# Kernel optimization log

Hardware: AMD Instinct MI355X
Metric: run time of the kernel (lower is better)

The kernel has to match this reference:

```python
import jax, jax.numpy as jnp
import numpy as np

H = 1024
NH = 16
DH = H // NH

def setup_inputs() -> dict:
    key = jax.random.key(0)
    ks = jax.random.split(key, 6)
    s = 1.0 / np.sqrt(H)
    x = jax.random.normal(ks[0], (4, 2048, H), dtype=jnp.float32)
    Wq = jax.random.uniform(ks[1], (H, H), jnp.float32, -s, s)
    Wk = jax.random.uniform(ks[2], (H, H), jnp.float32, -s, s)
    Wv = jax.random.uniform(ks[3], (H, H), jnp.float32, -s, s)
    Wo = jax.random.uniform(ks[4], (H, H), jnp.float32, -s, s)
    bo = jax.random.uniform(ks[5], (H,), jnp.float32, -s, s)
    return {"x": x, "Wq": Wq, "Wk": Wk, "Wv": Wv, "Wo": Wo, "bo": bo}

def reference(x, Wq, Wk, Wv, Wo, bo):
    B, T, Hd = x.shape
    # projections: torch Linear is x @ W.T
    def split_heads(y):
        return y.reshape(B, T, NH, DH).transpose(0, 2, 1, 3)  # [B, nh, T, dh]
    Q = split_heads(x @ Wq.T)
    K = split_heads(x @ Wk.T)
    V = split_heads(x @ Wv.T)
    scores = jnp.einsum('bhtd,bhsd->bhts', Q, K) / jnp.sqrt(jnp.float32(DH))
    w = jax.nn.softmax(scores, axis=-1)
    ctx = jnp.einsum('bhts,bhsd->bhtd', w, V)  # [B, nh, T, dh]
    ctx = ctx.transpose(0, 2, 1, 3).reshape(B, T, Hd)
    out = ctx @ Wo.T + bo  # [B, T, H]
    return out.mean(axis=1)  # [B, H]
```

## Files before the change

### kernel.cpp

```cpp
#include <hip/hip_runtime.h>
#include <hip/hip_bf16.h>
#include <cstdint>

#define BB   4
#define TT   2048
#define HH   1024
#define NHH  16
#define DHH  64
#define MM   (BB*TT)
#define N3   (3*HH)

typedef __attribute__((ext_vector_type(8))) short short8;
typedef __attribute__((ext_vector_type(4))) float f32x4;

__device__ __forceinline__ float bf2f(unsigned short u) {
    return __uint_as_float(((uint32_t)u) << 16);
}
__device__ __forceinline__ unsigned short f2bf(float f) {
    uint32_t u = __float_as_uint(f);
    return (unsigned short)((u + 0x7fffu + ((u >> 16) & 1u)) >> 16);
}
__device__ __forceinline__ void gload_lds16(const unsigned short* g, unsigned short* l) {
    __builtin_amdgcn_global_load_lds(
        (const __attribute__((address_space(1))) uint32_t*)g,
        (__attribute__((address_space(3))) uint32_t*)l, 16, 0, 0);
}

__global__ __launch_bounds__(256) void cvt_bf16(
    const float* __restrict__ src, unsigned short* __restrict__ dst, int n4)
{
    int i = blockIdx.x * 256 + threadIdx.x;
    const int stride = gridDim.x * 256;
    for (; i < n4; i += stride) {
        float4 v = ((const float4*)src)[i];
        ushort4 o;
        o.x = f2bf(v.x); o.y = f2bf(v.y); o.z = f2bf(v.z); o.w = f2bf(v.w);
        ((ushort4*)dst)[i] = o;
    }
}

__global__ __launch_bounds__(256) void proj_mfma(
    const unsigned short* __restrict__ xb, const unsigned short* __restrict__ Wb,
    unsigned short* __restrict__ C)
{
    __shared__ unsigned short As[4096];
    __shared__ unsigned short Bs[4096];
    const int m0 = blockIdx.x * 128;
    const int n0 = blockIdx.y * 128;
    const unsigned short* Wbase = Wb + (size_t)(n0 >> 10) * HH * HH;
    const int nw0 = n0 & (HH - 1);
    const int tid = threadIdx.x;
    const int wave = tid >> 6, lane = tid & 63;
    const int quad = lane >> 4, l15 = lane & 15;
    const int wm = wave >> 1, wn = wave & 1;

    f32x4 acc[4][4];
    #pragma unroll
    for (int i = 0; i < 4; ++i)
        #pragma unroll
        for (int j = 0; j < 4; ++j) acc[i][j] = (f32x4){0.f, 0.f, 0.f, 0.f};

    for (int k0 = 0; k0 < HH; k0 += 32) {
        __syncthreads();
        #pragma unroll
        for (int q = 0; q < 2; ++q) {
            const int chunk = (wave * 2 + q) * 64 + lane;
            const int kc = chunk >> 7, mrow = chunk & 127;
            gload_lds16(xb    + (size_t)(m0  + mrow) * HH + k0 + kc * 8, As + chunk * 8);
            gload_lds16(Wbase + (size_t)(nw0 + mrow) * HH + k0 + kc * 8, Bs + chunk * 8);
        }
        __syncthreads();
        short8 af[4], bf[4];
        #pragma unroll
        for (int i = 0; i < 4; ++i)
            af[i] = *(const short8*)&As[(quad * 128 + wm * 64 + i * 16 + l15) * 8];
        #pragma unroll
        for (int j = 0; j < 4; ++j)
            bf[j] = *(const short8*)&Bs[(quad * 128 + wn * 64 + j * 16 + l15) * 8];
        #pragma unroll
        for (int i = 0; i < 4; ++i)
            #pragma unroll
            for (int j = 0; j < 4; ++j)
                acc[i][j] = __builtin_amdgcn_mfma_f32_16x16x32_bf16(af[i], bf[j], acc[i][j], 0, 0, 0);
    }
    const float cscale = (n0 < HH) ? 0.125f : 1.0f;
    #pragma unroll
    for (int i = 0; i < 4; ++i)
        #pragma unroll
        for (int j = 0; j < 4; ++j) {
            const int col = n0 + wn * 64 + j * 16 + l15;
            #pragma unroll
            for (int r = 0; r < 4; ++r) {
                const int row = m0 + wm * 64 + i * 16 + quad * 4 + r;
                C[(size_t)row * N3 + col] = f2bf(acc[i][j][r] * cscale);
            }
        }
}

__global__ __launch_bounds__(256) void attn_fused(
    const unsigned short* __restrict__ qkv, float* __restrict__ a)
{
    const int t0 = blockIdx.x * 128;
    const int h = blockIdx.y, b = blockIdx.z;
    const int tid = threadIdx.x;
    const int wave = tid >> 6, lane = tid & 63;
    const int quad = lane >> 4, l15 = lane & 15;
    const int bh = b * NHH + h;
    __shared__ float red[4][128];
    __shared__ float linv[128];

    const size_t qbase = (size_t)(b * TT) * N3 + h * DHH;
    const size_t kbase = qbase + HH;

    short8 aq[8][2];
    #pragma unroll
    for (int i = 0; i < 8; ++i)
        #pragma unroll
        for (int c = 0; c < 2; ++c)
            aq[i][c] = *(const short8*)&qkv[qbase + (size_t)(t0 + i * 16 + l15) * N3 + quad * 8 + c * 32];

    float rs[8][4];
    #pragma unroll
    for (int i = 0; i < 8; ++i)
        #pragma unroll
        for (int r = 0; r < 4; ++r) rs[i][r] = 0.f;

    const size_t kstripe = kbase + (size_t)(wave * 512 + l15) * N3 + quad * 8;
    short8 nb0 = *(const short8*)&qkv[kstripe];
    short8 nb1 = *(const short8*)&qkv[kstripe + 32];
    for (int sstep = 0; sstep < 32; ++sstep) {
        const short8 bq0 = nb0, bq1 = nb1;
        if (sstep < 31) {
            const size_t krow = kstripe + (size_t)((sstep + 1) * 16) * N3;
            nb0 = *(const short8*)&qkv[krow];
            nb1 = *(const short8*)&qkv[krow + 32];
        }
        #pragma unroll
        for (int i = 0; i < 8; ++i) {
            f32x4 c = (f32x4){0.f, 0.f, 0.f, 0.f};
            c = __builtin_amdgcn_mfma_f32_16x16x32_bf16(aq[i][0], bq0, c, 0, 0, 0);
            c = __builtin_amdgcn_mfma_f32_16x16x32_bf16(aq[i][1], bq1, c, 0, 0, 0);
            #pragma unroll
            for (int r = 0; r < 4; ++r) rs[i][r] += __expf(c[r]);
        }
    }
    #pragma unroll
    for (int off = 1; off < 16; off <<= 1)
        #pragma unroll
        for (int i = 0; i < 8; ++i)
            #pragma unroll
            for (int r = 0; r < 4; ++r) rs[i][r] += __shfl_xor(rs[i][r], off);
    if (l15 == 0)
        #pragma unroll
        for (int i = 0; i < 8; ++i)
            #pragma unroll
            for (int r = 0; r < 4; ++r) red[wave][i * 16 + quad * 4 + r] = rs[i][r];
    __syncthreads();
    if (tid < 128) {
        const float l = red[0][tid] + red[1][tid] + red[2][tid] + red[3][tid];
        linv[tid] = 1.0f / (l * (float)TT);
    }
    __syncthreads();

    float lrv[8][4];
    #pragma unroll
    for (int i = 0; i < 8; ++i)
        #pragma unroll
        for (int r = 0; r < 4; ++r) lrv[i][r] = linv[i * 16 + quad * 4 + r];

    nb0 = *(const short8*)&qkv[kstripe];
    nb1 = *(const short8*)&qkv[kstripe + 32];
    for (int sstep = 0; sstep < 32; ++sstep) {
        const short8 bq0 = nb0, bq1 = nb1;
        if (sstep < 31) {
            const size_t krow = kstripe + (size_t)((sstep + 1) * 16) * N3;
            nb0 = *(const short8*)&qkv[krow];
            nb1 = *(const short8*)&qkv[krow + 32];
        }
        float cs = 0.f;
        #pragma unroll
        for (int i = 0; i < 8; ++i) {
            f32x4 c = (f32x4){0.f, 0.f, 0.f, 0.f};
            c = __builtin_amdgcn_mfma_f32_16x16x32_bf16(aq[i][0], bq0, c, 0, 0, 0);
            c = __builtin_amdgcn_mfma_f32_16x16x32_bf16(aq[i][1], bq1, c, 0, 0, 0);
            #pragma unroll
            for (int r = 0; r < 4; ++r) cs += __expf(c[r]) * lrv[i][r];
        }
        cs += __shfl_xor(cs, 16);
        cs += __shfl_xor(cs, 32);
        if (lane < 16)
            atomicAdd(&a[(size_t)bh * TT + wave * 512 + sstep * 16 + l15], cs);
    }
}

__global__ __launch_bounds__(256) void ctx_mean(
    const unsigned short* __restrict__ qkv, const float* __restrict__ a,
    float* __restrict__ cm)
{
    const int h = blockIdx.x, b = blockIdx.y, sb = blockIdx.z;
    const int tid = threadIdx.x;
    const int d = tid & 63, sg = tid >> 6;
    __shared__ float red[4][64];
    float part = 0.f;
    for (int s = sb * 256 + sg; s < sb * 256 + 256; s += 4) {
        const float av = a[(size_t)(b * NHH + h) * TT + s];
        part += av * bf2f(qkv[(size_t)(b * TT + s) * N3 + 2 * HH + h * DHH + d]);
    }
    red[sg][d] = part;
    __syncthreads();
    if (tid < 64)
        atomicAdd(&cm[b * HH + h * DHH + tid],
                  red[0][tid] + red[1][tid] + red[2][tid] + red[3][tid]);
}

__global__ __launch_bounds__(256) void out_proj(
    const float* __restrict__ cm, const float* __restrict__ Wo,
    const float* __restrict__ bo, float* __restrict__ out)
{
    const int b = blockIdx.y;
    const int jb = blockIdx.x;
    const int tid = threadIdx.x;
    const int j = jb * 64 + (tid >> 2);
    const int kg = tid & 3;
    __shared__ float cs[HH];
    for (int k = tid; k < HH; k += 256) cs[k] = cm[b * HH + k];
    __syncthreads();
    float acc = 0.f;
    const float* wrow = &Wo[(size_t)j * HH];
    #pragma unroll 8
    for (int i = 0; i < 64; ++i) {
        const int k = kg * 256 + i * 4;
        float4 w4 = *(const float4*)&wrow[k];
        acc += w4.x * cs[k] + w4.y * cs[k+1] + w4.z * cs[k+2] + w4.w * cs[k+3];
    }
    acc += __shfl_down(acc, 2, 4);
    acc += __shfl_down(acc, 1, 4);
    if (kg == 0) out[b * HH + j] = acc + bo[j];
}

extern "C" void kernel_launch(void* const* d_in, const int* in_sizes, int n_in,
                              void* d_out, int out_size, void* d_ws, size_t ws_size,
                              hipStream_t stream) {
    const float* x  = (const float*)d_in[0];
    const float* Wq = (const float*)d_in[1];
    const float* Wk = (const float*)d_in[2];
    const float* Wv = (const float*)d_in[3];
    const float* Wo = (const float*)d_in[4];
    const float* bo = (const float*)d_in[5];
    float* out = (float*)d_out;

    char* ws = (char*)d_ws;
    unsigned short* qkv = (unsigned short*)ws;
    ws += (size_t)MM * N3 * 2;
    unsigned short* xb = (unsigned short*)ws;
    ws += (size_t)MM * HH * 2;
    unsigned short* Wb = (unsigned short*)ws;
    ws += (size_t)3 * HH * HH * 2;
    float* a = (float*)ws;
    ws += (size_t)BB * NHH * TT * 4;
    float* cm = (float*)ws;

    hipMemsetAsync(a, 0, (size_t)(BB * NHH * TT + BB * HH) * 4, stream);

    cvt_bf16<<<2048, 256, 0, stream>>>(x,  xb,           MM * HH / 4);
    cvt_bf16<<<512,  256, 0, stream>>>(Wq, Wb,           HH * HH / 4);
    cvt_bf16<<<512,  256, 0, stream>>>(Wk, Wb + HH*HH,   HH * HH / 4);
    cvt_bf16<<<512,  256, 0, stream>>>(Wv, Wb + 2*HH*HH, HH * HH / 4);

    proj_mfma <<<dim3(64, 24),      256, 0, stream>>>(xb, Wb, qkv);
    attn_fused<<<dim3(16, NHH, BB), 256, 0, stream>>>(qkv, a);
    ctx_mean  <<<dim3(NHH, BB, 8),  256, 0, stream>>>(qkv, a, cm);
    out_proj  <<<dim3(16, BB),      256, 0, stream>>>(cm, Wo, bo, out);
}
```

Before: 335.5 us.

## Store Q/K/V head-major, use exp2 with folded log2e scale, deepen K prefetch

The projection epilogue now writes Q, K and V into separate [B,NH,T,DH] buffers instead of one interleaved [M,3H] matrix, so the attention and ctx kernels read contiguous per-head rows. The Q scale folds in log2(e), which lets the softmax use the hardware exp2 instead of __expf. The K register prefetch is deepened to two steps ahead, and the three weight conversions are merged into one launch. In exchange, the projection's scattered epilogue stores may coalesce less well, and the extra prefetch registers raise register pressure.

```diff
diff --git a/kernel.cpp b/kernel.cpp
--- a/kernel.cpp
+++ b/kernel.cpp
@@ -13,6 +13,14 @@
 typedef __attribute__((ext_vector_type(8))) short short8;
 typedef __attribute__((ext_vector_type(4))) float f32x4;
 
+#if __has_builtin(__builtin_amdgcn_exp2f)
+#define EXP2F(x) __builtin_amdgcn_exp2f(x)
+#else
+#define EXP2F(x) exp2f(x)
+#endif
+
+#define QSCALE 0.1803368801111204f
+
 __device__ __forceinline__ float bf2f(unsigned short u) {
     return __uint_as_float(((uint32_t)u) << 16);
 }
@@ -39,15 +47,34 @@
     }
 }
 
+__global__ __launch_bounds__(256) void cvt_w3(
+    const float* __restrict__ Wq, const float* __restrict__ Wk,
+    const float* __restrict__ Wv, unsigned short* __restrict__ Wb)
+{
+    const float* src = (blockIdx.y == 0) ? Wq : (blockIdx.y == 1 ? Wk : Wv);
+    unsigned short* dst = Wb + (size_t)blockIdx.y * HH * HH;
+    const int n4 = HH * HH / 4;
+    int i = blockIdx.x * 256 + threadIdx.x;
+    const int stride = gridDim.x * 256;
+    for (; i < n4; i += stride) {
+        float4 v = ((const float4*)src)[i];
+        ushort4 o;
+        o.x = f2bf(v.x); o.y = f2bf(v.y); o.z = f2bf(v.z); o.w = f2bf(v.w);
+        ((ushort4*)dst)[i] = o;
+    }
+}
+
 __global__ __launch_bounds__(256) void proj_mfma(
     const unsigned short* __restrict__ xb, const unsigned short* __restrict__ Wb,
-    unsigned short* __restrict__ C)
+    unsigned short* __restrict__ qp, unsigned short* __restrict__ kp,
+    unsigned short* __restrict__ vp)
 {
     __shared__ unsigned short As[4096];
     __shared__ unsigned short Bs[4096];
     const int m0 = blockIdx.x * 128;
     const int n0 = blockIdx.y * 128;
-    const unsigned short* Wbase = Wb + (size_t)(n0 >> 10) * HH * HH;
+    const int sel = n0 >> 10;
+    const unsigned short* Wbase = Wb + (size_t)sel * HH * HH;
     const int nw0 = n0 & (HH - 1);
     const int tid = threadIdx.x;
     const int wave = tid >> 6, lane = tid & 63;
@@ -83,41 +110,50 @@
             for (int j = 0; j < 4; ++j)
                 acc[i][j] = __builtin_amdgcn_mfma_f32_16x16x32_bf16(af[i], bf[j], acc[i][j], 0, 0, 0);
     }
-    const float cscale = (n0 < HH) ? 0.125f : 1.0f;
+    unsigned short* outp = (sel == 0) ? qp : (sel == 1 ? kp : vp);
+    const float cscale = (sel == 0) ? QSCALE : 1.0f;
     #pragma unroll
     for (int i = 0; i < 4; ++i)
         #pragma unroll
         for (int j = 0; j < 4; ++j) {
             const int col = n0 + wn * 64 + j * 16 + l15;
+            const int hh2 = (col >> 6) & (NHH - 1);
+            const int dd  = col & (DHH - 1);
             #pragma unroll
             for (int r = 0; r < 4; ++r) {
                 const int row = m0 + wm * 64 + i * 16 + quad * 4 + r;
-                C[(size_t)row * N3 + col] = f2bf(acc[i][j][r] * cscale);
+                const int bb2 = row >> 11, tt2 = row & (TT - 1);
+                outp[((size_t)(bb2 * NHH + hh2) * TT + tt2) * DHH + dd] =
+                    f2bf(acc[i][j][r] * cscale);
             }
         }
 }
 
 __global__ __launch_bounds__(256) void attn_fused(
-    const unsigned short* __restrict__ qkv, float* __restrict__ a)
+    const unsigned short* __restrict__ qp, const unsigned short* __restrict__ kp,
+    float* __restrict__ a)
 {
     const int t0 = blockIdx.x * 128;
     const int h = blockIdx.y, b = blockIdx.z;
+    const int bh = b * NHH + h;
     const int tid = threadIdx.x;
     const int wave = tid >> 6, lane = tid & 63;
     const int quad = lane >> 4, l15 = lane & 15;
-    const int bh = b * NHH + h;
     __shared__ float red[4][128];
     __shared__ float linv[128];
 
-    const size_t qbase = (size_t)(b * TT) * N3 + h * DHH;
-    const size_t kbase = qbase + HH;
+    const unsigned short* q = qp + (size_t)bh * TT * DHH;
+    const unsigned short* kptr =
+        kp + (size_t)bh * TT * DHH + (size_t)(wave * 512 + l15) * DHH + quad * 8;
 
     short8 aq[8][2];
     #pragma unroll
     for (int i = 0; i < 8; ++i)
         #pragma unroll
         for (int c = 0; c < 2; ++c)
-            aq[i][c] = *(const short8*)&qkv[qbase + (size_t)(t0 + i * 16 + l15) * N3 + quad * 8 + c * 32];
+            aq[i][c] = *(const short8*)&q[(size_t)(t0 + i * 16 + l15) * DHH + quad * 8 + c * 32];
+
+#define KLD(ss, c) (*(const short8*)(kptr + (size_t)(ss) * 16 * DHH + (c) * 32))
 
     float rs[8][4];
     #pragma unroll
@@ -125,23 +161,21 @@
         #pragma unroll
         for (int r = 0; r < 4; ++r) rs[i][r] = 0.f;
 
-    const size_t kstripe = kbase + (size_t)(wave * 512 + l15) * N3 + quad * 8;
-    short8 nb0 = *(const short8*)&qkv[kstripe];
-    short8 nb1 = *(const short8*)&qkv[kstripe + 32];
-    for (int sstep = 0; sstep < 32; ++sstep) {
-        const short8 bq0 = nb0, bq1 = nb1;
-        if (sstep < 31) {
-            const size_t krow = kstripe + (size_t)((sstep + 1) * 16) * N3;
-            nb0 = *(const short8*)&qkv[krow];
-            nb1 = *(const short8*)&qkv[krow + 32];
-        }
-        #pragma unroll
-        for (int i = 0; i < 8; ++i) {
-            f32x4 c = (f32x4){0.f, 0.f, 0.f, 0.f};
-            c = __builtin_amdgcn_mfma_f32_16x16x32_bf16(aq[i][0], bq0, c, 0, 0, 0);
-            c = __builtin_amdgcn_mfma_f32_16x16x32_bf16(aq[i][1], bq1, c, 0, 0, 0);
-            #pragma unroll
-            for (int r = 0; r < 4; ++r) rs[i][r] += __expf(c[r]);
+    {
+        short8 c0a = KLD(0, 0), c0b = KLD(0, 1);
+        short8 c1a = KLD(1, 0), c1b = KLD(1, 1);
+        for (int ss = 0; ss < 32; ++ss) {
+            const short8 ba = c0a, bb = c0b;
+            c0a = c1a; c0b = c1b;
+            if (ss < 30) { c1a = KLD(ss + 2, 0); c1b = KLD(ss + 2, 1); }
+            #pragma unroll
+            for (int i = 0; i < 8; ++i) {
+                f32x4 c = (f32x4){0.f, 0.f, 0.f, 0.f};
+                c = __builtin_amdgcn_mfma_f32_16x16x32_bf16(aq[i][0], ba, c, 0, 0, 0);
+                c = __builtin_amdgcn_mfma_f32_16x16x32_bf16(aq[i][1], bb, c, 0, 0, 0);
+                #pragma unroll
+                for (int r = 0; r < 4; ++r) rs[i][r] += EXP2F(c[r]);
+            }
         }
     }
     #pragma unroll
@@ -168,43 +202,44 @@
         #pragma unroll
         for (int r = 0; r < 4; ++r) lrv[i][r] = linv[i * 16 + quad * 4 + r];
 
-    nb0 = *(const short8*)&qkv[kstripe];
-    nb1 = *(const short8*)&qkv[kstripe + 32];
-    for (int sstep = 0; sstep < 32; ++sstep) {
-        const short8 bq0 = nb0, bq1 = nb1;
-        if (sstep < 31) {
-            const size_t krow = kstripe + (size_t)((sstep + 1) * 16) * N3;
-            nb0 = *(const short8*)&qkv[krow];
-            nb1 = *(const short8*)&qkv[krow + 32];
+    {
+        short8 c0a = KLD(0, 0), c0b = KLD(0, 1);
+        short8 c1a = KLD(1, 0), c1b = KLD(1, 1);
+        for (int ss = 0; ss < 32; ++ss) {
+            const short8 ba = c0a, bb = c0b;
+            c0a = c1a; c0b = c1b;
+            if (ss < 30) { c1a = KLD(ss + 2, 0); c1b = KLD(ss + 2, 1); }
+            float cs = 0.f;
+            #pragma unroll
+            for (int i = 0; i < 8; ++i) {
+                f32x4 c = (f32x4){0.f, 0.f, 0.f, 0.f};
+                c = __builtin_amdgcn_mfma_f32_16x16x32_bf16(aq[i][0], ba, c, 0, 0, 0);
+                c = __builtin_amdgcn_mfma_f32_16x16x32_bf16(aq[i][1], bb, c, 0, 0, 0);
+                #pragma unroll
+                for (int r = 0; r < 4; ++r) cs += EXP2F(c[r]) * lrv[i][r];
+            }
+            cs += __shfl_xor(cs, 16);
+            cs += __shfl_xor(cs, 32);
+            if (lane < 16)
+                atomicAdd(&a[(size_t)bh * TT + wave * 512 + ss * 16 + l15], cs);
         }
-        float cs = 0.f;
-        #pragma unroll
-        for (int i = 0; i < 8; ++i) {
-            f32x4 c = (f32x4){0.f, 0.f, 0.f, 0.f};
-            c = __builtin_amdgcn_mfma_f32_16x16x32_bf16(aq[i][0], bq0, c, 0, 0, 0);
-            c = __builtin_amdgcn_mfma_f32_16x16x32_bf16(aq[i][1], bq1, c, 0, 0, 0);
-            #pragma unroll
-            for (int r = 0; r < 4; ++r) cs += __expf(c[r]) * lrv[i][r];
-        }
-        cs += __shfl_xor(cs, 16);
-        cs += __shfl_xor(cs, 32);
-        if (lane < 16)
-            atomicAdd(&a[(size_t)bh * TT + wave * 512 + sstep * 16 + l15], cs);
-    }
+    }
+#undef KLD
 }
 
 __global__ __launch_bounds__(256) void ctx_mean(
-    const unsigned short* __restrict__ qkv, const float* __restrict__ a,
+    const unsigned short* __restrict__ vp, const float* __restrict__ a,
     float* __restrict__ cm)
 {
     const int h = blockIdx.x, b = blockIdx.y, sb = blockIdx.z;
     const int tid = threadIdx.x;
     const int d = tid & 63, sg = tid >> 6;
+    const int bh = b * NHH + h;
     __shared__ float red[4][64];
     float part = 0.f;
     for (int s = sb * 256 + sg; s < sb * 256 + 256; s += 4) {
-        const float av = a[(size_t)(b * NHH + h) * TT + s];
-        part += av * bf2f(qkv[(size_t)(b * TT + s) * N3 + 2 * HH + h * DHH + d]);
+        const float av = a[(size_t)bh * TT + s];
+        part += av * bf2f(vp[((size_t)bh * TT + s) * DHH + d]);
     }
     red[sg][d] = part;
     __syncthreads();
@@ -250,25 +285,21 @@
     float* out = (float*)d_out;
 
     char* ws = (char*)d_ws;
-    unsigned short* qkv = (unsigned short*)ws;
-    ws += (size_t)MM * N3 * 2;
-    unsigned short* xb = (unsigned short*)ws;
-    ws += (size_t)MM * HH * 2;
-    unsigned short* Wb = (unsigned short*)ws;
-    ws += (size_t)3 * HH * HH * 2;
-    float* a = (float*)ws;
-    ws += (size_t)BB * NHH * TT * 4;
+    unsigned short* qp = (unsigned short*)ws;  ws += (size_t)MM * HH * 2;
+    unsigned short* kp = (unsigned short*)ws;  ws += (size_t)MM * HH * 2;
+    unsigned short* vp = (unsigned short*)ws;  ws += (size_t)MM * HH * 2;
+    unsigned short* xb = (unsigned short*)ws;  ws += (size_t)MM * HH * 2;
+    unsigned short* Wb = (unsigned short*)ws;  ws += (size_t)3 * HH * HH * 2;
+    float* a  = (float*)ws;                    ws += (size_t)BB * NHH * TT * 4;
     float* cm = (float*)ws;
 
     hipMemsetAsync(a, 0, (size_t)(BB * NHH * TT + BB * HH) * 4, stream);
 
-    cvt_bf16<<<2048, 256, 0, stream>>>(x,  xb,           MM * HH / 4);
-    cvt_bf16<<<512,  256, 0, stream>>>(Wq, Wb,           HH * HH / 4);
-    cvt_bf16<<<512,  256, 0, stream>>>(Wk, Wb + HH*HH,   HH * HH / 4);
-    cvt_bf16<<<512,  256, 0, stream>>>(Wv, Wb + 2*HH*HH, HH * HH / 4);
-
-    proj_mfma <<<dim3(64, 24),      256, 0, stream>>>(xb, Wb, qkv);
-    attn_fused<<<dim3(16, NHH, BB), 256, 0, stream>>>(qkv, a);
-    ctx_mean  <<<dim3(NHH, BB, 8),  256, 0, stream>>>(qkv, a, cm);
+    cvt_bf16<<<2048, 256, 0, stream>>>(x, xb, MM * HH / 4);
+    cvt_w3  <<<dim3(512, 3), 256, 0, stream>>>(Wq, Wk, Wv, Wb);
+
+    proj_mfma <<<dim3(64, 24),      256, 0, stream>>>(xb, Wb, qp, kp, vp);
+    attn_fused<<<dim3(16, NHH, BB), 256, 0, stream>>>(qp, kp, a);
+    ctx_mean  <<<dim3(NHH, BB, 8),  256, 0, stream>>>(vp, a, cm);
     out_proj  <<<dim3(16, BB),      256, 0, stream>>>(cm, Wo, bo, out);
 }
```

New measurement: 321.2 us. 4.3% less time.
